# Optimization experiments

Hardware: AMD Instinct MI355X
Metric: run time of the kernel (lower is better)

The kernel has to match this reference:

```python
import jax, jax.numpy as jnp
import numpy as np

FEATURE_DIM = 2048
LABEL_DIM = 80
EMBED_DIM = 512
OUTPUT_DIM = 2048
NUM_EXPERTS = 8
BATCH = 1024
IN_DIM = FEATURE_DIM + EMBED_DIM


def setup_inputs() -> dict:
    key = jax.random.key(0)
    ks = jax.random.split(key, 7)
    features = jax.random.normal(ks[0], (BATCH, FEATURE_DIM), dtype=jnp.float32)
    labels = jax.random.uniform(ks[1], (BATCH, LABEL_DIM), dtype=jnp.float32)
    # learned parameters
    label_embed = jax.random.normal(ks[2], (LABEL_DIM, EMBED_DIM), dtype=jnp.float32)
    gate_w = jax.random.normal(ks[3], (IN_DIM, NUM_EXPERTS), dtype=jnp.float32) * (1.0 / np.sqrt(IN_DIM))
    gate_b = jnp.zeros((NUM_EXPERTS,), dtype=jnp.float32)
    expert_w = jax.random.normal(ks[4], (NUM_EXPERTS, IN_DIM, OUTPUT_DIM), dtype=jnp.float32) * (1.0 / np.sqrt(IN_DIM))
    expert_b = jnp.zeros((NUM_EXPERTS, OUTPUT_DIM), dtype=jnp.float32)
    return {
        "features": features,
        "labels": labels,
        "label_embed": label_embed,
        "gate_w": gate_w,
        "gate_b": gate_b,
        "expert_w": expert_w,
        "expert_b": expert_b,
    }


def reference(features, labels, label_embed, gate_w, gate_b, expert_w, expert_b):
    # labels: [B, L] soft multilabel -> label embedding mix [B, E]
    label_embeds = labels @ label_embed                      # [B, EMBED_DIM]
    combined = jnp.concatenate([features, label_embeds], axis=-1)  # [B, IN_DIM]
    gating = jax.nn.sigmoid(combined @ gate_w + gate_b)      # [B, NUM_EXPERTS]
    # all-experts batched GEMM: [B, IN] x [E, IN, OUT] -> [B, E, OUT]
    expert_out = jnp.einsum('bi,eio->beo', combined, expert_w) + expert_b[None, :, :]
    # gate-weighted reduction over experts
    out = jnp.einsum('be,beo->bo', gating, expert_out)       # [B, OUT]
    return out
```

## Files before the change

### kernel.cpp

```cpp
#include <hip/hip_runtime.h>
#include <hip/hip_bf16.h>

#define BATCH   1024
#define FDIM    2048
#define LDIM    80
#define EDIM    512
#define ODIM    2048
#define NEXP    8
#define INDIM   2560

#define BM      256
#define BN      256
#define BK      64
#define NKT     (INDIM / BK)

typedef __bf16 bf16x8 __attribute__((ext_vector_type(8)));
typedef float  f32x4  __attribute__((ext_vector_type(4)));

__device__ __forceinline__ unsigned int pack2(float lo, float hi) {
    __hip_bfloat162 h = __float22bfloat162_rn(make_float2(lo, hi));
    unsigned int u;
    __builtin_memcpy(&u, &h, 4);
    return u;
}
__device__ __forceinline__ float bf2f(unsigned short h) {
    return __uint_as_float((unsigned int)h << 16);
}
__device__ __forceinline__ void gload_lds16(const void* g, void* l) {
    __builtin_amdgcn_global_load_lds(
        (__attribute__((address_space(1))) void*)g,
        (__attribute__((address_space(3))) void*)l,
        16, 0, 0);
}

#define BAR()       __builtin_amdgcn_s_barrier()
#define SCHED_PIN() __builtin_amdgcn_sched_barrier(0)

#define CW_TK 64
#define CW_TO 128
#define CW_BLOCKS  ((ODIM / CW_TO) * (INDIM / CW_TK) * NEXP)
#define PREP_BLOCKS (BATCH / 4)
#define GATE_BLOCKS (BATCH)
#define FRONT_BLOCKS (CW_BLOCKS + PREP_BLOCKS + GATE_BLOCKS)

__global__ __launch_bounds__(256) void front_kernel(
    const float* __restrict__ W, unsigned short* __restrict__ Wb,
    const float* __restrict__ features, const float* __restrict__ labels,
    const float* __restrict__ label_embed, unsigned short* __restrict__ cb,
    const float* __restrict__ gw, const float* __restrict__ gb,
    float* __restrict__ gating)
{
    __shared__ float smem[CW_TK * CW_TO];
    const int bid = blockIdx.x;
    const int t   = threadIdx.x;

    if (bid >= PREP_BLOCKS + GATE_BLOCKS) {
        const int cwb = bid - (PREP_BLOCKS + GATE_BLOCKS);
        const int o0 = (cwb & 15) * CW_TO;
        const int k0 = ((cwb >> 4) % (INDIM / CW_TK)) * CW_TK;
        const int e  = cwb / ((ODIM / CW_TO) * (INDIM / CW_TK));

        const int rowi = t >> 5;
        const int ch   = t & 31;
        const float* srcbase = W + (size_t)e * ((size_t)INDIM * ODIM)
                                 + (size_t)k0 * ODIM + o0;
        float* ldsbase = smem + (t >> 6) * 256;
        #pragma unroll
        for (int p = 0; p < 8; ++p) {
            gload_lds16(srcbase + (size_t)(p * 8 + rowi) * ODIM + ch * 4,
                        ldsbase + p * 1024);
        }
        __syncthreads();

        const int o = t >> 1;
        const int h = t & 1;
        unsigned short* dst = Wb + (size_t)e * ((size_t)ODIM * INDIM)
                                 + (size_t)(o0 + o) * INDIM + k0 + h * 32;
        #pragma unroll
        for (int u = 0; u < 4; ++u) {
            const int kb = h * 32 + u * 8;
            const float* col = smem + (size_t)kb * 128 + o;
            unsigned int w0 = pack2(col[0 * 128], col[1 * 128]);
            unsigned int w1 = pack2(col[2 * 128], col[3 * 128]);
            unsigned int w2 = pack2(col[4 * 128], col[5 * 128]);
            unsigned int w3 = pack2(col[6 * 128], col[7 * 128]);
            ((uint4*)dst)[u] = make_uint4(w0, w1, w2, w3);
        }
    } else if (bid < PREP_BLOCKS) {
        const int b0 = bid * 4;
        float (*lab)[LDIM] = (float(*)[LDIM])smem;
        for (int idx = t; idx < 4 * LDIM; idx += 256) {
            lab[idx / LDIM][idx % LDIM] = labels[(size_t)(b0 + idx / LDIM) * LDIM + (idx % LDIM)];
        }
        __syncthreads();
        {
            const int r = t >> 6, c64 = t & 63;
            const float4* F4 = (const float4*)features;
            #pragma unroll
            for (int ch = 0; ch < 8; ++ch) {
                float4 v = F4[(size_t)(b0 + r) * (FDIM / 4) + c64 + 64 * ch];
                uint2 pk;
                pk.x = pack2(v.x, v.y);
                pk.y = pack2(v.z, v.w);
                *(uint2*)(cb + (size_t)(b0 + r) * INDIM + (size_t)(c64 + 64 * ch) * 4) = pk;
            }
        }
        {
            const int j = 2 * t;
            float acc[4][2] = {{0,0},{0,0},{0,0},{0,0}};
            const float2* le2 = (const float2*)label_embed;
            for (int l = 0; l < LDIM; ++l) {
                float2 le = le2[(size_t)l * (EDIM / 2) + t];
                #pragma unroll
                for (int r = 0; r < 4; ++r) {
                    float lv = lab[r][l];
                    acc[r][0] += lv * le.x;
                    acc[r][1] += lv * le.y;
                }
            }
            #pragma unroll
            for (int r = 0; r < 4; ++r) {
                *(unsigned int*)(cb + (size_t)(b0 + r) * INDIM + FDIM + j) = pack2(acc[r][0], acc[r][1]);
            }
        }
    } else {
        const int b = bid - PREP_BLOCKS;
        float* labs = smem;
        float (*red)[NEXP] = (float(*)[NEXP])(smem + 128);
        if (t < LDIM) labs[t] = labels[(size_t)b * LDIM + t];
        __syncthreads();

        float p[NEXP] = {0,0,0,0,0,0,0,0};
        for (int i = t; i < FDIM; i += 256) {
            float c = features[(size_t)b * FDIM + i];
            const float4* g4 = (const float4*)(gw + (size_t)i * NEXP);
            float4 u = g4[0], v = g4[1];
            p[0] += c * u.x; p[1] += c * u.y; p[2] += c * u.z; p[3] += c * u.w;
            p[4] += c * v.x; p[5] += c * v.y; p[6] += c * v.z; p[7] += c * v.w;
        }
        float le0 = 0.f, le1 = 0.f;
        #pragma unroll 8
        for (int l = 0; l < LDIM; ++l) {
            float lv = labs[l];
            le0 += lv * label_embed[(size_t)l * EDIM + t];
            le1 += lv * label_embed[(size_t)l * EDIM + t + 256];
        }
        {
            const float4* g4 = (const float4*)(gw + (size_t)(FDIM + t) * NEXP);
            float4 u = g4[0], v = g4[1];
            p[0] += le0 * u.x; p[1] += le0 * u.y; p[2] += le0 * u.z; p[3] += le0 * u.w;
            p[4] += le0 * v.x; p[5] += le0 * v.y; p[6] += le0 * v.z; p[7] += le0 * v.w;
            const float4* g5 = (const float4*)(gw + (size_t)(FDIM + 256 + t) * NEXP);
            float4 u2 = g5[0], v2 = g5[1];
            p[0] += le1 * u2.x; p[1] += le1 * u2.y; p[2] += le1 * u2.z; p[3] += le1 * u2.w;
            p[4] += le1 * v2.x; p[5] += le1 * v2.y; p[6] += le1 * v2.z; p[7] += le1 * v2.w;
        }
        const int lane = t & 63, wave = t >> 6;
        #pragma unroll
        for (int e = 0; e < NEXP; ++e) {
            float v = p[e];
            v += __shfl_down(v, 32); v += __shfl_down(v, 16); v += __shfl_down(v, 8);
            v += __shfl_down(v, 4);  v += __shfl_down(v, 2);  v += __shfl_down(v, 1);
            if (lane == 0) red[wave][e] = v;
        }
        __syncthreads();
        if (t < NEXP) {
            float s = red[0][t] + red[1][t] + red[2][t] + red[3][t] + gb[t];
            gating[(size_t)b * NEXP + t] = 1.0f / (1.0f + __expf(-s));
        }
    }
}

__global__ __launch_bounds__(256) void prep_kernel(
    const float* __restrict__ features, const float* __restrict__ labels,
    const float* __restrict__ label_embed, unsigned short* __restrict__ cb)
{
    const int b0 = blockIdx.x * 4;
    const int t  = threadIdx.x;
    __shared__ float lab[4][LDIM];
    for (int idx = t; idx < 4 * LDIM; idx += 256) {
        lab[idx / LDIM][idx % LDIM] = labels[(size_t)(b0 + idx / LDIM) * LDIM + (idx % LDIM)];
    }
    __syncthreads();

    {
        const int r = t >> 6, c64 = t & 63;
        const float4* F4 = (const float4*)features;
        #pragma unroll
        for (int ch = 0; ch < 8; ++ch) {
            float4 v = F4[(size_t)(b0 + r) * (FDIM / 4) + c64 + 64 * ch];
            uint2 pk;
            pk.x = pack2(v.x, v.y);
            pk.y = pack2(v.z, v.w);
            *(uint2*)(cb + (size_t)(b0 + r) * INDIM + (size_t)(c64 + 64 * ch) * 4) = pk;
        }
    }
    {
        const int j = 2 * t;
        float acc[4][2] = {{0,0},{0,0},{0,0},{0,0}};
        const float2* le2 = (const float2*)label_embed;
        for (int l = 0; l < LDIM; ++l) {
            float2 le = le2[(size_t)l * (EDIM / 2) + t];
            #pragma unroll
            for (int r = 0; r < 4; ++r) {
                float lv = lab[r][l];
                acc[r][0] += lv * le.x;
                acc[r][1] += lv * le.y;
            }
        }
        #pragma unroll
        for (int r = 0; r < 4; ++r) {
            *(unsigned int*)(cb + (size_t)(b0 + r) * INDIM + FDIM + j) = pack2(acc[r][0], acc[r][1]);
        }
    }
}

__global__ __launch_bounds__(256) void gate_kernel(
    const unsigned short* __restrict__ cb, const float* __restrict__ gw,
    const float* __restrict__ gb, float* __restrict__ gating)
{
    const int b = blockIdx.x, t = threadIdx.x;
    float p[NEXP] = {0,0,0,0,0,0,0,0};
    for (int i = t; i < INDIM; i += 256) {
        float c = bf2f(cb[(size_t)b * INDIM + i]);
        const float4* g4 = (const float4*)(gw + (size_t)i * NEXP);
        float4 u = g4[0], v = g4[1];
        p[0] += c * u.x; p[1] += c * u.y; p[2] += c * u.z; p[3] += c * u.w;
        p[4] += c * v.x; p[5] += c * v.y; p[6] += c * v.z; p[7] += c * v.w;
    }
    __shared__ float red[4][NEXP];
    const int lane = t & 63, wave = t >> 6;
    #pragma unroll
    for (int e = 0; e < NEXP; ++e) {
        float v = p[e];
        v += __shfl_down(v, 32); v += __shfl_down(v, 16); v += __shfl_down(v, 8);
        v += __shfl_down(v, 4);  v += __shfl_down(v, 2);  v += __shfl_down(v, 1);
        if (lane == 0) red[wave][e] = v;
    }
    __syncthreads();
    if (t < NEXP) {
        float s = red[0][t] + red[1][t] + red[2][t] + red[3][t] + gb[t];
        gating[(size_t)b * NEXP + t] = 1.0f / (1.0f + __expf(-s));
    }
}

template<bool ATOMIC>
__global__ __launch_bounds__(512, 2) void moe_gemm8(
    const unsigned short* __restrict__ cb, const unsigned short* __restrict__ Wb,
    const float* __restrict__ gating, const float* __restrict__ eb,
    float* __restrict__ dst)
{
    __shared__ unsigned short As0[256 * 64];
    __shared__ unsigned short Bs0[256 * 64];
    __shared__ unsigned short As1[256 * 64];
    __shared__ unsigned short Bs1[256 * 64];

    const int t = threadIdx.x;
    const int lane = t & 63, wave = t >> 6;
    const int n0 = blockIdx.x * BN;
    const int m0 = blockIdx.y * BM;
    const int e  = blockIdx.z;

    const int wmi = wave >> 2;
    const int wni = wave & 3;
    const int wmBase = wmi * 128;
    const int wnBase = wni * 64;
    const int fm = lane & 15, fq = lane >> 4;
    const int fsw = fm & 7;

    const int srow = t >> 3;
    const int scn  = (t & 7) ^ (srow & 7);
    const size_t gOff = (size_t)srow * INDIM + (size_t)scn * 8;
    const unsigned short* aS = cb + (size_t)m0 * INDIM + gOff;
    const unsigned short* bS = Wb + (size_t)e * ((size_t)ODIM * INDIM)
                                  + (size_t)n0 * INDIM + gOff;

    #define STAGE4_A(DST, kt) { _Pragma("unroll") for (int q = 0; q < 4; ++q) \
        gload_lds16(aS + (size_t)q * (64 * INDIM) + (size_t)(kt) * 64, (DST) + q * 4096 + wave * 512); }
    #define STAGE4_B(DST, kt) { _Pragma("unroll") for (int q = 0; q < 4; ++q) \
        gload_lds16(bS + (size_t)q * (64 * INDIM) + (size_t)(kt) * 64, (DST) + q * 4096 + wave * 512); }

    #define PH_READ_A(RA, base) { _Pragma("unroll") for (int mi = 0; mi < 4; ++mi) \
        _Pragma("unroll") for (int ks = 0; ks < 2; ++ks) \
            af[mi][ks] = *(const bf16x8*)((RA) + (wmBase + (base) + mi * 16 + fm) * 64 \
                                               + (((ks * 4 + fq) ^ fsw) * 8)); }
    #define PH_READ_B(BF, RB, base) { _Pragma("unroll") for (int ni = 0; ni < 2; ++ni) \
        _Pragma("unroll") for (int ks = 0; ks < 2; ++ks) \
            BF[ni][ks] = *(const bf16x8*)((RB) + (wnBase + (base) + ni * 16 + fm) * 64 \
                                               + (((ks * 4 + fq) ^ fsw) * 8)); }
    #define MFMA16(AI, AJ, BF) { __builtin_amdgcn_s_setprio(1); \
        _Pragma("unroll") for (int mi = 0; mi < 4; ++mi) \
        _Pragma("unroll") for (int ni = 0; ni < 2; ++ni) \
        _Pragma("unroll") for (int ks = 0; ks < 2; ++ks) \
            acc[(AI) + mi][(AJ) + ni] = __builtin_amdgcn_mfma_f32_16x16x32_bf16( \
                af[mi][ks], BF[ni][ks], acc[(AI) + mi][(AJ) + ni], 0, 0, 0); \
        __builtin_amdgcn_s_setprio(0); }

    f32x4 acc[8][4];
    #pragma unroll
    for (int i = 0; i < 8; ++i)
        #pragma unroll
        for (int j = 0; j < 4; ++j) acc[i][j] = (f32x4){0.f, 0.f, 0.f, 0.f};

    bf16x8 af[4][2], bA[2][2], bB[2][2];

    STAGE4_A(As0, 0); STAGE4_B(Bs0, 0); STAGE4_B(Bs1, 1);
    asm volatile("s_waitcnt vmcnt(4)");
    BAR(); SCHED_PIN();

    #define TILE(kt, RA, RB, OA) { \
         \
        PH_READ_A(RA, 0); \
        PH_READ_B(bA, RB, 0); \
        if ((kt) + 1 < NKT) STAGE4_A(OA, (kt) + 1); \
        BAR(); \
        MFMA16(0, 0, bA); \
        SCHED_PIN(); BAR(); SCHED_PIN(); \
         \
        PH_READ_B(bB, RB, 32); \
        BAR(); \
        MFMA16(0, 2, bB); \
        SCHED_PIN(); BAR(); SCHED_PIN(); \
         \
        PH_READ_A(RA, 64); \
        BAR(); \
        MFMA16(4, 2, bB); \
        SCHED_PIN(); BAR(); SCHED_PIN(); \
         \
        if ((kt) + 2 < NKT) STAGE4_B(RB, (kt) + 2); \
        BAR(); \
        MFMA16(4, 0, bA); \
        SCHED_PIN(); \
        if ((kt) + 2 < NKT) { asm volatile("s_waitcnt vmcnt(4)"); } \
        else                { asm volatile("s_waitcnt vmcnt(0)"); } \
        BAR(); SCHED_PIN(); \
    }

    for (int kt = 0; kt < NKT; kt += 2) {
        TILE(kt,     As0, Bs0, As1);
        TILE(kt + 1, As1, Bs1, As0);
    }
    #undef TILE
    #undef STAGE4_A
    #undef STAGE4_B
    #undef PH_READ_A
    #undef PH_READ_B
    #undef MFMA16

    #pragma unroll
    for (int mi = 0; mi < 8; ++mi) {
        const int grow = m0 + wmBase + mi * 16 + fq * 4;
        const float g0 = gating[(size_t)(grow + 0) * NEXP + e];
        const float g1 = gating[(size_t)(grow + 1) * NEXP + e];
        const float g2 = gating[(size_t)(grow + 2) * NEXP + e];
        const float g3 = gating[(size_t)(grow + 3) * NEXP + e];
        #pragma unroll
        for (int ni = 0; ni < 4; ++ni) {
            const int gcol = n0 + wnBase + ni * 16 + fm;
            const float bias = eb[(size_t)e * ODIM + gcol];
            f32x4 a = acc[mi][ni];
            if (ATOMIC) {
                unsafeAtomicAdd(dst + (size_t)(grow + 0) * ODIM + gcol, g0 * (a.x + bias));
                unsafeAtomicAdd(dst + (size_t)(grow + 1) * ODIM + gcol, g1 * (a.y + bias));
                unsafeAtomicAdd(dst + (size_t)(grow + 2) * ODIM + gcol, g2 * (a.z + bias));
                unsafeAtomicAdd(dst + (size_t)(grow + 3) * ODIM + gcol, g3 * (a.w + bias));
            } else {
                float* pd = dst + ((size_t)e * BATCH + grow) * ODIM + gcol;
                pd[0 * ODIM] = g0 * (a.x + bias);
                pd[1 * ODIM] = g1 * (a.y + bias);
                pd[2 * ODIM] = g2 * (a.z + bias);
                pd[3 * ODIM] = g3 * (a.w + bias);
            }
        }
    }
}

__global__ __launch_bounds__(256) void combine_kernel(
    const float* __restrict__ parts, float* __restrict__ out)
{
    const int idx = blockIdx.x * 256 + threadIdx.x;
    const float4* p = (const float4*)parts;
    float4 s = p[idx];
    #pragma unroll
    for (int e = 1; e < NEXP; ++e) {
        float4 v = p[(size_t)e * (BATCH * ODIM / 4) + idx];
        s.x += v.x; s.y += v.y; s.z += v.z; s.w += v.w;
    }
    ((float4*)out)[idx] = s;
}

__global__ __launch_bounds__(256) void moe_gemm_slow(
    const unsigned short* __restrict__ cb, const float* __restrict__ W,
    const float* __restrict__ gating, const float* __restrict__ eb,
    float* __restrict__ out)
{
    __shared__ unsigned short As[128 * 32];
    __shared__ unsigned short Bs[128 * 32];

    const int t = threadIdx.x;
    const int lane = t & 63, wave = t >> 6;
    const int n0 = blockIdx.x * 128;
    const int m0 = blockIdx.y * 128;
    const int e  = blockIdx.z;

    f32x4 acc[4][4];
    #pragma unroll
    for (int i = 0; i < 4; ++i)
        #pragma unroll
        for (int j = 0; j < 4; ++j) acc[i][j] = (f32x4){0.f, 0.f, 0.f, 0.f};

    const int arow = t >> 2, acg = t & 3;
    const unsigned short* ag0 = cb + (size_t)(m0 + arow) * INDIM + acg * 8;
    unsigned short* al0 = As + wave * 512;
    unsigned short* al1 = As + 2048 + wave * 512;

    const int bg = t & 15;
    const int bu = t >> 4;
    const float* wg = W + (size_t)e * ((size_t)INDIM * ODIM) + (size_t)(2 * bg) * ODIM + n0 + bu * 8;
    unsigned int* bl = (unsigned int*)Bs + bg + bu * 128;

    const int fm = lane & 15, fq = lane >> 4;
    const int wn = (wave & 1) * 64;
    const int wm = (wave >> 1) * 64;

    for (int k0 = 0; k0 < INDIM; k0 += 32) {
        __syncthreads();
        gload_lds16(ag0 + k0, al0);
        gload_lds16(ag0 + (size_t)64 * INDIM + k0, al1);
        const float* wp = wg + (size_t)k0 * ODIM;
        float4 r0a = *(const float4*)(wp);
        float4 r0b = *(const float4*)(wp + 4);
        float4 r1a = *(const float4*)(wp + ODIM);
        float4 r1b = *(const float4*)(wp + ODIM + 4);
        bl[0 * 16] = pack2(r0a.x, r1a.x);
        bl[1 * 16] = pack2(r0a.y, r1a.y);
        bl[2 * 16] = pack2(r0a.z, r1a.z);
        bl[3 * 16] = pack2(r0a.w, r1a.w);
        bl[4 * 16] = pack2(r0b.x, r1b.x);
        bl[5 * 16] = pack2(r0b.y, r1b.y);
        bl[6 * 16] = pack2(r0b.z, r1b.z);
        bl[7 * 16] = pack2(r0b.w, r1b.w);
        __syncthreads();

        bf16x8 af[4], bfr[4];
        #pragma unroll
        for (int mi = 0; mi < 4; ++mi)
            af[mi] = *(const bf16x8*)(As + (wm + mi * 16 + fm) * 32 + fq * 8);
        #pragma unroll
        for (int ni = 0; ni < 4; ++ni)
            bfr[ni] = *(const bf16x8*)(Bs + (wn + ni * 16 + fm) * 32 + fq * 8);
        #pragma unroll
        for (int mi = 0; mi < 4; ++mi)
            #pragma unroll
            for (int ni = 0; ni < 4; ++ni)
                acc[mi][ni] = __builtin_amdgcn_mfma_f32_16x16x32_bf16(af[mi], bfr[ni], acc[mi][ni], 0, 0, 0);
    }

    #pragma unroll
    for (int mi = 0; mi < 4; ++mi) {
        const int grow = m0 + wm + mi * 16 + fq * 4;
        const float g0 = gating[(size_t)(grow + 0) * NEXP + e];
        const float g1 = gating[(size_t)(grow + 1) * NEXP + e];
        const float g2 = gating[(size_t)(grow + 2) * NEXP + e];
        const float g3 = gating[(size_t)(grow + 3) * NEXP + e];
        #pragma unroll
        for (int ni = 0; ni < 4; ++ni) {
            const int gcol = n0 + wn + ni * 16 + fm;
            const float bias = eb[(size_t)e * ODIM + gcol];
            f32x4 a = acc[mi][ni];
            unsafeAtomicAdd(out + (size_t)(grow + 0) * ODIM + gcol, g0 * (a.x + bias));
            unsafeAtomicAdd(out + (size_t)(grow + 1) * ODIM + gcol, g1 * (a.y + bias));
            unsafeAtomicAdd(out + (size_t)(grow + 2) * ODIM + gcol, g2 * (a.z + bias));
            unsafeAtomicAdd(out + (size_t)(grow + 3) * ODIM + gcol, g3 * (a.w + bias));
        }
    }
}

extern "C" void kernel_launch(void* const* d_in, const int* in_sizes, int n_in,
                              void* d_out, int out_size, void* d_ws, size_t ws_size,
                              hipStream_t stream) {
    const float* features    = (const float*)d_in[0];
    const float* labels      = (const float*)d_in[1];
    const float* label_embed = (const float*)d_in[2];
    const float* gate_w      = (const float*)d_in[3];
    const float* gate_b      = (const float*)d_in[4];
    const float* expert_w    = (const float*)d_in[5];
    const float* expert_b    = (const float*)d_in[6];
    float* out = (float*)d_out;

    const size_t wb_bytes = (size_t)NEXP * ODIM * INDIM * 2;
    const size_t cb_bytes = (size_t)BATCH * INDIM * 2;
    const size_t gt_bytes = (size_t)BATCH * NEXP * 4;
    const size_t pt_bytes = (size_t)NEXP * BATCH * ODIM * 4;
    const bool fast  = ws_size >= wb_bytes + cb_bytes + gt_bytes;
    const bool fast2 = ws_size >= wb_bytes + cb_bytes + gt_bytes + pt_bytes;

    if (fast) {
        unsigned short* Wb = (unsigned short*)d_ws;
        unsigned short* cb = (unsigned short*)((char*)d_ws + wb_bytes);
        float* gating = (float*)((char*)d_ws + wb_bytes + cb_bytes);
        float* parts  = (float*)((char*)d_ws + wb_bytes + cb_bytes + gt_bytes);
        front_kernel<<<FRONT_BLOCKS, 256, 0, stream>>>(
            expert_w, Wb, features, labels, label_embed, cb, gate_w, gate_b, gating);
        if (fast2) {
            moe_gemm8<false><<<dim3(ODIM / BN, BATCH / BM, NEXP), 512, 0, stream>>>(cb, Wb, gating, expert_b, parts);
            combine_kernel<<<(BATCH * ODIM / 4) / 256, 256, 0, stream>>>(parts, out);
        } else {
            hipMemsetAsync(d_out, 0, (size_t)BATCH * ODIM * sizeof(float), stream);
            moe_gemm8<true><<<dim3(ODIM / BN, BATCH / BM, NEXP), 512, 0, stream>>>(cb, Wb, gating, expert_b, out);
        }
    } else {
        unsigned short* cb = (unsigned short*)d_ws;
        float* gating = (float*)((char*)d_ws + cb_bytes);
        hipMemsetAsync(d_out, 0, (size_t)BATCH * ODIM * sizeof(float), stream);
        prep_kernel<<<BATCH / 4, 256, 0, stream>>>(features, labels, label_embed, cb);
        gate_kernel<<<BATCH, 256, 0, stream>>>(cb, gate_w, gate_b, gating);
        moe_gemm_slow<<<dim3(ODIM / 128, BATCH / 128, NEXP), 256, 0, stream>>>(cb, expert_w, gating, expert_b, out);
    }
}
```

Before: 372.3 us.

## Split tile global-to-LDS loads into half-quadrant groups across MFMA phases

Result: no change. 371.8 us (-0.1%).

```diff
diff --git a/kernel.cpp b/kernel.cpp
--- a/kernel.cpp
+++ b/kernel.cpp
@@ -275,10 +275,12 @@
     const unsigned short* bS = Wb + (size_t)e * ((size_t)ODIM * INDIM)
                                   + (size_t)n0 * INDIM + gOff;
 
-    #define STAGE4_A(DST, kt) { _Pragma("unroll") for (int q = 0; q < 4; ++q) \
-        gload_lds16(aS + (size_t)q * (64 * INDIM) + (size_t)(kt) * 64, (DST) + q * 4096 + wave * 512); }
-    #define STAGE4_B(DST, kt) { _Pragma("unroll") for (int q = 0; q < 4; ++q) \
-        gload_lds16(bS + (size_t)q * (64 * INDIM) + (size_t)(kt) * 64, (DST) + q * 4096 + wave * 512); }
+    #define STAGE_A2Q(DST, kt, qa, qb) { \
+        gload_lds16(aS + (size_t)(qa) * (64 * INDIM) + (size_t)(kt) * 64, (DST) + (qa) * 4096 + wave * 512); \
+        gload_lds16(aS + (size_t)(qb) * (64 * INDIM) + (size_t)(kt) * 64, (DST) + (qb) * 4096 + wave * 512); }
+    #define STAGE_B2Q(DST, kt, qa, qb) { \
+        gload_lds16(bS + (size_t)(qa) * (64 * INDIM) + (size_t)(kt) * 64, (DST) + (qa) * 4096 + wave * 512); \
+        gload_lds16(bS + (size_t)(qb) * (64 * INDIM) + (size_t)(kt) * 64, (DST) + (qb) * 4096 + wave * 512); }
 
     #define PH_READ_A(RA, base) { _Pragma("unroll") for (int mi = 0; mi < 4; ++mi) \
         _Pragma("unroll") for (int ks = 0; ks < 2; ++ks) \
@@ -304,45 +306,50 @@
 
     bf16x8 af[4][2], bA[2][2], bB[2][2];
 
-    STAGE4_A(As0, 0); STAGE4_B(Bs0, 0); STAGE4_B(Bs1, 1);
-    asm volatile("s_waitcnt vmcnt(4)");
+    STAGE_A2Q(As0, 0, 0, 1); STAGE_A2Q(As0, 0, 2, 3);
+    STAGE_B2Q(Bs0, 0, 0, 1); STAGE_B2Q(Bs0, 0, 2, 3);
+    STAGE_B2Q(Bs1, 1, 0, 1); STAGE_B2Q(Bs1, 1, 2, 3);
+    STAGE_A2Q(As1, 1, 0, 2);
+    asm volatile("s_waitcnt vmcnt(6)");
     BAR(); SCHED_PIN();
 
-    #define TILE(kt, RA, RB, OA) { \
+    #define TILE(kt, RA, RB, OA, OB) { \
          \
         PH_READ_A(RA, 0); \
         PH_READ_B(bA, RB, 0); \
-        if ((kt) + 1 < NKT) STAGE4_A(OA, (kt) + 1); \
+        if ((kt) + 1 < NKT) STAGE_A2Q(OA, (kt) + 1, 1, 3); \
         BAR(); \
         MFMA16(0, 0, bA); \
         SCHED_PIN(); BAR(); SCHED_PIN(); \
          \
         PH_READ_B(bB, RB, 32); \
+        if ((kt) + 2 < NKT) STAGE_A2Q(RA, (kt) + 2, 0, 2); \
         BAR(); \
         MFMA16(0, 2, bB); \
         SCHED_PIN(); BAR(); SCHED_PIN(); \
          \
         PH_READ_A(RA, 64); \
+        if ((kt) + 2 < NKT) STAGE_B2Q(RB, (kt) + 2, 0, 1); \
         BAR(); \
         MFMA16(4, 2, bB); \
         SCHED_PIN(); BAR(); SCHED_PIN(); \
          \
-        if ((kt) + 2 < NKT) STAGE4_B(RB, (kt) + 2); \
+        if ((kt) + 2 < NKT) STAGE_B2Q(RB, (kt) + 2, 2, 3); \
         BAR(); \
         MFMA16(4, 0, bA); \
         SCHED_PIN(); \
-        if ((kt) + 2 < NKT) { asm volatile("s_waitcnt vmcnt(4)"); } \
+        if ((kt) + 2 < NKT) { asm volatile("s_waitcnt vmcnt(6)"); } \
         else                { asm volatile("s_waitcnt vmcnt(0)"); } \
         BAR(); SCHED_PIN(); \
     }
 
     for (int kt = 0; kt < NKT; kt += 2) {
-        TILE(kt,     As0, Bs0, As1);
-        TILE(kt + 1, As1, Bs1, As0);
+        TILE(kt,     As0, Bs0, As1, Bs1);
+        TILE(kt + 1, As1, Bs1, As0, Bs0);
     }
     #undef TILE
-    #undef STAGE4_A
-    #undef STAGE4_B
+    #undef STAGE_A2Q
+    #undef STAGE_B2Q
     #undef PH_READ_A
     #undef PH_READ_B
     #undef MFMA16
```
